# Kernel tuning notes

Hardware: AMD Instinct MI355X
Metric: run time of the kernel (lower is better)

The kernel has to match this reference:

```python
import jax, jax.numpy as jnp
import numpy as np

B, T, D, H, L, V = 4, 512, 512, 8, 8, 32000
HS = D // H
DF = 4 * D
EPS = 1e-5


def setup_inputs() -> dict:
    key = jax.random.key(0)
    ks = jax.random.split(key, 16)
    p = lambda k, s: jax.random.normal(k, s, jnp.float32) * 0.02
    return {
        'idx': jax.random.randint(ks[0], (B, T), 0, V),
        'targets': jax.random.randint(ks[1], (B, T), 0, V),
        'tok_emb': p(ks[2], (V, D)),
        'pos_emb': p(ks[3], (T, D)),
        'un_qkv_w': p(ks[4], (L, 3, D, D)),
        'un_qkv_b': jnp.zeros((L, 3, D), jnp.float32),
        'un_proj_w': p(ks[5], (L, D, D)),
        'un_proj_b': jnp.zeros((L, D), jnp.float32),
        'm_qkv_w': p(ks[6], (L, 3, D, D)),
        'm_qkv_b': jnp.zeros((L, 3, D), jnp.float32),
        'm_proj_w': p(ks[7], (L, D, D)),
        'm_proj_b': jnp.zeros((L, D), jnp.float32),
        'ff_w1': p(ks[8], (L, D, DF)),
        'ff_b1': jnp.zeros((L, DF), jnp.float32),
        'ff_w2': p(ks[9], (L, DF, D)),
        'ff_b2': jnp.zeros((L, D), jnp.float32),
        'ln1_g': jnp.ones((L, D), jnp.float32),
        'ln1_b': jnp.zeros((L, D), jnp.float32),
        'ln2_g': jnp.ones((L, D), jnp.float32),
        'ln2_b': jnp.zeros((L, D), jnp.float32),
        'lnf_g': jnp.ones((D,), jnp.float32),
        'lnf_b': jnp.zeros((D,), jnp.float32),
        'w_out': p(ks[10], (D, V)),
        'b_out': jnp.zeros((V,), jnp.float32),
    }


def _ln(x, g, b):
    mu = jnp.mean(x, -1, keepdims=True)
    var = jnp.var(x, -1, keepdims=True)
    return (x - mu) * jax.lax.rsqrt(var + EPS) * g + b


def _mha(x, qkv_w, qkv_b, pw, pb, mask):
    b, t, _ = x.shape
    # per-head linears concatenated == single D->D linear split into heads
    qkv = jnp.einsum('btd,cdf->cbtf', x, qkv_w) + qkv_b[:, None, None, :]
    q, k, v = (a.reshape(b, t, H, HS).transpose(0, 2, 1, 3) for a in qkv)
    w = jnp.einsum('bhtd,bhsd->bhts', q, k) * (HS ** -0.5)
    if mask is not None:
        w = jnp.where(mask, w, -jnp.inf)
    w = jax.nn.softmax(w, -1)  # dropout is identity in eval
    o = jnp.einsum('bhts,bhsd->bhtd', w, v).transpose(0, 2, 1, 3).reshape(b, t, D)
    return o @ pw + pb


def _ff(x, w1, b1, w2, b2):
    return jax.nn.gelu(x @ w1 + b1, approximate=False) @ w2 + b2


def _forward(idx, targets, tok_emb, pos_emb, layer_params, lnf_g, lnf_b, w_out, b_out):
    b, t = idx.shape
    x = tok_emb[idx] + pos_emb[:t]
    tril = jnp.tril(jnp.ones((t, t), bool))[None, None]

    def step(x, p):
        (uqw, uqb, upw, upb, mqw, mqb, mpw, mpb,
         w1, b1, w2, b2, g1, bb1, g2, bb2) = p
        # Block.forward (norm1/norm2/ffwd params are reused twice, as in source)
        x2 = x + _mha(_ln(x, g1, bb1), uqw, uqb, upw, upb, None)
        x = x2 + _ff(_ln(x2, g2, bb2), w1, b1, w2, b2)
        x2 = x + _mha(_ln(x, g1, bb1), mqw, mqb, mpw, mpb, tril)
        x = x2 + _ff(_ln(x2, g2, bb2), w1, b1, w2, b2)
        return x, None

    x, _ = jax.lax.scan(step, x, layer_params)
    x = _ln(x, lnf_g, lnf_b)
    logits = x @ w_out + b_out
    lsm = jax.nn.log_softmax(logits, -1)
    loss = -jnp.take_along_axis(lsm, targets[..., None], -1).mean()
    return logits, loss


def reference(idx, targets, tok_emb, pos_emb, un_qkv_w, un_qkv_b, un_proj_w,
              un_proj_b, m_qkv_w, m_qkv_b, m_proj_w, m_proj_b, ff_w1, ff_b1,
              ff_w2, ff_b2, ln1_g, ln1_b, ln2_g, ln2_b, lnf_g, lnf_b, w_out,
              b_out):
    layer_params = (un_qkv_w, un_qkv_b, un_proj_w, un_proj_b, m_qkv_w, m_qkv_b,
                    m_proj_w, m_proj_b, ff_w1, ff_b1, ff_w2, ff_b2, ln1_g,
                    ln1_b, ln2_g, ln2_b)
    return _forward(idx, targets, tok_emb, pos_emb, layer_params, lnf_g,
                    lnf_b, w_out, b_out)
```

## Files before the change

kernel.cpp:

```cpp
#include <hip/hip_runtime.h>

typedef unsigned short u16;
typedef __bf16 bf16x8 __attribute__((ext_vector_type(8)));
typedef float f32x4 __attribute__((ext_vector_type(4)));
typedef u16 u16x8 __attribute__((ext_vector_type(8)));

#define DEVINL __device__ __forceinline__

static constexpr int Tn  = 512;
static constexpr int Dn  = 512;
static constexpr int Hn  = 8;
static constexpr int HSn = 64;
static constexpr int Vn  = 32000;
static constexpr int Lnum = 8;
static constexpr int DFn = 2048;
static constexpr int BTn = 2048;

DEVINL u16 f2bf(float f) {
  unsigned u = __float_as_uint(f);
  u += 0x7fffu + ((u >> 16) & 1u);
  return (u16)(u >> 16);
}

DEVINL void gl_lds16(const u16* src, u16* dst) {
  __builtin_amdgcn_global_load_lds(
      (const __attribute__((address_space(1))) unsigned int*)src,
      (__attribute__((address_space(3))) unsigned int*)dst, 16, 0, 0);
}

__global__ __launch_bounds__(256) void transpose_w(const float* __restrict__ in,
                                                   u16* __restrict__ out,
                                                   int R, int C) {
  __shared__ float tile[32][33];
  long zoff = (long)blockIdx.z * R * C;
  int c0 = blockIdx.x * 32, r0 = blockIdx.y * 32;
  for (int e = threadIdx.x; e < 1024; e += 256) {
    int r = e >> 5, c = e & 31;
    tile[r][c] = in[zoff + (long)(r0 + r) * C + (c0 + c)];
  }
  __syncthreads();
  for (int e = threadIdx.x; e < 1024; e += 256) {
    int c = e >> 5, r = e & 31;
    out[zoff + (long)(c0 + c) * R + (r0 + r)] = f2bf(tile[r][c]);
  }
}

__global__ __launch_bounds__(256) void embed_kernel(const int* __restrict__ idx,
                                                    const float* __restrict__ tok,
                                                    const float* __restrict__ pos,
                                                    float* __restrict__ x) {
  int i = blockIdx.x * 256 + threadIdx.x;
  int bt = i >> 7;
  int d4 = (i & 127) * 4;
  int t = bt & (Tn - 1);
  long tk = (long)idx[bt] * Dn + d4;
  f32x4 a = *(const f32x4*)(tok + tk);
  f32x4 p = *(const f32x4*)(pos + (long)t * Dn + d4);
  a = a + p;
  *(f32x4*)(x + (long)bt * Dn + d4) = a;
}

__global__ __launch_bounds__(256) void ln_kernel(const float* __restrict__ x,
                                                 const float* __restrict__ g,
                                                 const float* __restrict__ b,
                                                 u16* __restrict__ out) {
  int lane = threadIdx.x & 63, wid = threadIdx.x >> 6;
  long row = (long)blockIdx.x * 4 + wid;
  const float* xr = x + row * Dn;
  f32x4 v0 = *(const f32x4*)(xr + lane * 8);
  f32x4 v1 = *(const f32x4*)(xr + lane * 8 + 4);
  float s = v0[0] + v0[1] + v0[2] + v0[3] + v1[0] + v1[1] + v1[2] + v1[3];
  float s2 = v0[0]*v0[0] + v0[1]*v0[1] + v0[2]*v0[2] + v0[3]*v0[3]
           + v1[0]*v1[0] + v1[1]*v1[1] + v1[2]*v1[2] + v1[3]*v1[3];
#pragma unroll
  for (int o = 32; o; o >>= 1) { s += __shfl_xor(s, o); s2 += __shfl_xor(s2, o); }
  float mu = s * (1.f / Dn);
  float rv = rsqrtf(s2 * (1.f / Dn) - mu * mu + 1e-5f);
  u16x8 o8;
#pragma unroll
  for (int j = 0; j < 8; ++j) {
    int c = lane * 8 + j;
    float xv = (j < 4) ? v0[j] : v1[j - 4];
    o8[j] = f2bf((xv - mu) * rv * g[c] + b[c]);
  }
  *(u16x8*)(out + row * Dn + lane * 8) = o8;
}

template<int BM, int BN, bool BIAS, bool RES, bool GELU, bool OBF, bool LOSSP>
__global__ __launch_bounds__(256, 2)
void gemm_kernel(const u16* __restrict__ A, const u16* __restrict__ B,
                 const float* __restrict__ bias, const float* __restrict__ res,
                 void* __restrict__ Cptr, int M, int N, int K, int ldc,
                 long aBatch, long bBatch, int zdiv, long zs1, long zs2,
                 float* __restrict__ lossP) {
  constexpr int BK = 32;
  constexpr int FM = BM / 32, FN = BN / 32;
  __shared__ __align__(16) u16 lds[2][(BM + BN) * BK];
  const int tid = threadIdx.x, lane = tid & 63, wid = tid >> 6;
  const int z = blockIdx.z;
  const u16* Ab = A + (long)z * aBatch + (long)blockIdx.y * BM * K;
  const u16* Bb = B + (long)z * bBatch + (long)blockIdx.x * BN * K;
  const int wr = wid >> 1, wc = wid & 1;
  const int r16 = lane & 15, kg = lane >> 4;

  f32x4 acc[FM][FN];
#pragma unroll
  for (int i = 0; i < FM; ++i)
#pragma unroll
    for (int j = 0; j < FN; ++j) acc[i][j] = (f32x4){0.f, 0.f, 0.f, 0.f};

  auto stage = [&](int buf, int kt) {
#pragma unroll
    for (int i = 0; i < BM / 64; ++i) {
      int fr = i * 4 + wid;
      const u16* src = Ab + (long)(fr * 16 + r16) * K + kt * BK + kg * 8;
      gl_lds16(src, &lds[buf][(i * 4 + wid) * 512]);
    }
#pragma unroll
    for (int i = 0; i < BN / 64; ++i) {
      int fr = i * 4 + wid;
      const u16* src = Bb + (long)(fr * 16 + r16) * K + kt * BK + kg * 8;
      gl_lds16(src, &lds[buf][BM * BK + (i * 4 + wid) * 512]);
    }
  };

  const int NT = K / BK;
  stage(0, 0);
  int cur = 0;
  for (int kt = 0; kt < NT; ++kt) {
    __syncthreads();
    if (kt + 1 < NT) stage(cur ^ 1, kt + 1);
    const u16* la = &lds[cur][0];
    const u16* lb = &lds[cur][BM * BK];
    bf16x8 af[FM], bfr[FN];
#pragma unroll
    for (int mi = 0; mi < FM; ++mi)
      af[mi] = *(const bf16x8*)(la + ((wr * FM + mi) * 64 + lane) * 8);
#pragma unroll
    for (int ni = 0; ni < FN; ++ni)
      bfr[ni] = *(const bf16x8*)(lb + ((wc * FN + ni) * 64 + lane) * 8);
#pragma unroll
    for (int mi = 0; mi < FM; ++mi)
#pragma unroll
      for (int ni = 0; ni < FN; ++ni)
        acc[mi][ni] = __builtin_amdgcn_mfma_f32_16x16x32_bf16(
            af[mi], bfr[ni], acc[mi][ni], 0, 0, 0);
    cur ^= 1;
  }

  if (LOSSP) {
#pragma unroll
    for (int mi = 0; mi < FM; ++mi) {
      float vals[FN][4];
#pragma unroll
      for (int ni = 0; ni < FN; ++ni) {
        int col = blockIdx.x * BN + wc * (BN / 2) + ni * 16 + r16;
        float bv = bias[col];
#pragma unroll
        for (int r = 0; r < 4; ++r) {
          int row = blockIdx.y * BM + wr * (BM / 2) + mi * 16 + kg * 4 + r;
          float v = acc[mi][ni][r] + bv;
          ((float*)Cptr)[(long)row * ldc + col] = v;
          vals[ni][r] = v;
        }
      }
#pragma unroll
      for (int r = 0; r < 4; ++r) {
        float mx = vals[0][r];
#pragma unroll
        for (int ni = 1; ni < FN; ++ni) mx = fmaxf(mx, vals[ni][r]);
#pragma unroll
        for (int off = 1; off < 16; off <<= 1) mx = fmaxf(mx, __shfl_xor(mx, off));
        float s = 0.f;
#pragma unroll
        for (int ni = 0; ni < FN; ++ni) s += __expf(vals[ni][r] - mx);
#pragma unroll
        for (int off = 1; off < 16; off <<= 1) s += __shfl_xor(s, off);
        if (r16 == 0) {
          int row = blockIdx.y * BM + wr * (BM / 2) + mi * 16 + kg * 4 + r;
          int grp = blockIdx.x * (BN / 64) + wc;
          float2* pp = (float2*)lossP;
          pp[(long)row * (Vn / 64) + grp] = make_float2(mx, s);
        }
      }
    }
    return;
  }

  long cOff = (long)(z / zdiv) * zs1 + (long)(z % zdiv) * zs2;
#pragma unroll
  for (int mi = 0; mi < FM; ++mi) {
#pragma unroll
    for (int ni = 0; ni < FN; ++ni) {
      int col = blockIdx.x * BN + wc * (BN / 2) + ni * 16 + r16;
      float bv = 0.f;
      if (BIAS) bv = bias[col];
#pragma unroll
      for (int r = 0; r < 4; ++r) {
        int row = blockIdx.y * BM + wr * (BM / 2) + mi * 16 + kg * 4 + r;
        float v = acc[mi][ni][r] + bv;
        if (GELU) v = 0.5f * v * (1.f + erff(v * 0.70710678f));
        long ci = cOff + (long)row * ldc + col;
        if (RES) v += res[ci];
        if (OBF) ((u16*)Cptr)[ci] = f2bf(v);
        else     ((float*)Cptr)[ci] = v;
      }
    }
  }
}

__global__ __launch_bounds__(256) void qkv_split(const u16* __restrict__ qkv,
                                                 u16* __restrict__ q,
                                                 u16* __restrict__ k,
                                                 u16* __restrict__ vT) {
  __shared__ u16 vt[32][72];
  int bh = blockIdx.y, b = bh >> 3, h = bh & 7;
  int t0 = blockIdx.x * 32;
  for (int e = threadIdx.x; e < 2048; e += 256) {
    int tt = e >> 6, d = e & 63;
    long src = ((long)(b * Tn + t0 + tt)) * (3 * Dn) + h * HSn + d;
    long dst = ((long)bh * Tn + t0 + tt) * HSn + d;
    q[dst] = qkv[src];
    k[dst] = qkv[src + Dn];
    vt[tt][d] = qkv[src + 2 * Dn];
  }
  __syncthreads();
  for (int e = threadIdx.x; e < 2048; e += 256) {
    int d = e >> 5, tt = e & 31;
    vT[((long)bh * HSn + d) * Tn + t0 + tt] = vt[tt][d];
  }
}

template<int CAUSAL>
__global__ __launch_bounds__(256, 2)
void flash_kernel(const u16* __restrict__ qb, const u16* __restrict__ kb,
                  const u16* __restrict__ vTb, u16* __restrict__ ob) {
  __shared__ __align__(16) u16 Qs[8 * 512];
  __shared__ __align__(16) u16 Ks[16 * 512];
  __shared__ __align__(16) u16 Vs[16 * 512];
  __shared__ __align__(16) u16 Ps[16 * 512];
  const int tid = threadIdx.x, lane = tid & 63, w = tid >> 6;
  const int r16 = lane & 15, kg = lane >> 4;
  const int bh = blockIdx.y, qt = blockIdx.x, q0 = qt * 64;
  const long bhT = (long)bh * Tn;

#pragma unroll
  for (int ks = 0; ks < 2; ++ks) {
    const u16* src = qb + (bhT + q0 + w * 16 + r16) * 64 + ks * 32 + kg * 8;
    gl_lds16(src, Qs + (ks * 4 + w) * 512);
  }

  f32x4 acc_o[4];
#pragma unroll
  for (int fd = 0; fd < 4; ++fd) acc_o[fd] = (f32x4){0.f, 0.f, 0.f, 0.f};
  float m[4], l[4];
#pragma unroll
  for (int r = 0; r < 4; ++r) { m[r] = -1e30f; l[r] = 0.f; }

  const int nt = CAUSAL ? (qt >> 1) + 1 : 4;
  for (int it = 0; it < nt; ++it) {
    const int kt0 = it * 128;
    __syncthreads();
#pragma unroll
    for (int j = 0; j < 4; ++j) {
      int idx = j * 4 + w;
      int ks = idx >> 3, fn = idx & 7;
      const u16* src = kb + (bhT + kt0 + fn * 16 + r16) * 64 + ks * 32 + kg * 8;
      gl_lds16(src, Ks + idx * 512);
    }
#pragma unroll
    for (int j = 0; j < 4; ++j) {
      int idx = j * 4 + w;
      int ks = idx >> 2, fn = idx & 3;
      const u16* src = vTb + ((long)bh * 64 + fn * 16 + r16) * 512 + kt0 + ks * 32 + kg * 8;
      gl_lds16(src, Vs + idx * 512);
    }
    __syncthreads();

    f32x4 sa[8];
#pragma unroll
    for (int fn = 0; fn < 8; ++fn) sa[fn] = (f32x4){0.f, 0.f, 0.f, 0.f};
#pragma unroll
    for (int ks = 0; ks < 2; ++ks) {
      bf16x8 aq = *(const bf16x8*)(Qs + (ks * 4 + w) * 512 + lane * 8);
#pragma unroll
      for (int fn = 0; fn < 8; ++fn)
        sa[fn] = __builtin_amdgcn_mfma_f32_16x16x32_bf16(
            aq, *(const bf16x8*)(Ks + (ks * 8 + fn) * 512 + lane * 8), sa[fn], 0, 0, 0);
    }

    const bool masked = CAUSAL && (it == nt - 1);
#pragma unroll
    for (int r = 0; r < 4; ++r) {
      float sv[8];
      float mx = -1e30f;
      int qv = q0 + w * 16 + kg * 4 + r;
#pragma unroll
      for (int fn = 0; fn < 8; ++fn) {
        float vv = sa[fn][r] * 0.125f;
        if (masked) {
          int ktv = kt0 + fn * 16 + r16;
          if (ktv > qv) vv = -1e30f;
        }
        sv[fn] = vv;
        mx = fmaxf(mx, vv);
      }
#pragma unroll
      for (int off = 1; off < 16; off <<= 1) mx = fmaxf(mx, __shfl_xor(mx, off));
      float nm = fmaxf(m[r], mx);
      float sc = __expf(m[r] - nm);
      float rs = 0.f;
#pragma unroll
      for (int fn = 0; fn < 8; ++fn) { float p = __expf(sv[fn] - nm); sv[fn] = p; rs += p; }
#pragma unroll
      for (int off = 1; off < 16; off <<= 1) rs += __shfl_xor(rs, off);
      l[r] = l[r] * sc + rs;
      m[r] = nm;
#pragma unroll
      for (int fd = 0; fd < 4; ++fd) acc_o[fd][r] *= sc;
#pragma unroll
      for (int fn = 0; fn < 8; ++fn) {
        int t = fn * 16 + r16;
        int q = kg * 4 + r;
        Ps[w * 2048 + (t >> 5) * 512 + ((t >> 3) & 3) * 128 + q * 8 + (t & 7)] = f2bf(sv[fn]);
      }
    }

#pragma unroll
    for (int ks = 0; ks < 4; ++ks) {
      bf16x8 pa = *(const bf16x8*)(Ps + w * 2048 + ks * 512 + lane * 8);
#pragma unroll
      for (int fd = 0; fd < 4; ++fd)
        acc_o[fd] = __builtin_amdgcn_mfma_f32_16x16x32_bf16(
            pa, *(const bf16x8*)(Vs + (ks * 4 + fd) * 512 + lane * 8), acc_o[fd], 0, 0, 0);
    }
  }

  const int b = bh >> 3, h = bh & 7;
#pragma unroll
  for (int fd = 0; fd < 4; ++fd) {
#pragma unroll
    for (int r = 0; r < 4; ++r) {
      int q = q0 + w * 16 + kg * 4 + r;
      int d = fd * 16 + r16;
      ob[((long)(b * Tn + q)) * Dn + h * 64 + d] = f2bf(acc_o[fd][r] / l[r]);
    }
  }
}

__global__ __launch_bounds__(256) void loss_combine(const float* __restrict__ lossP,
                                                    const float* __restrict__ logits,
                                                    const int* __restrict__ targets,
                                                    float* __restrict__ loss) {
  int w = threadIdx.x >> 6, lane = threadIdx.x & 63;
  int row = blockIdx.x * 4 + w;
  const float2* lp = (const float2*)lossP + (long)row * (Vn / 64);
  float m = -1e30f, s = 0.f;
  for (int e = lane; e < Vn / 64; e += 64) {
    float2 p = lp[e];
    float nm = fmaxf(m, p.x);
    s = s * __expf(m - nm) + p.y * __expf(p.x - nm);
    m = nm;
  }
#pragma unroll
  for (int off = 1; off < 64; off <<= 1) {
    float om = __shfl_xor(m, off), os = __shfl_xor(s, off);
    float nm = fmaxf(m, om);
    s = s * __expf(m - nm) + os * __expf(om - nm);
    m = nm;
  }
  if (lane == 0) {
    float lse = m + logf(s);
    float nll = lse - logits[(long)row * Vn + targets[row]];
    atomicAdd(loss, nll * (1.f / BTn));
  }
}

extern "C" void kernel_launch(void* const* d_in, const int* in_sizes, int n_in,
                              void* d_out, int out_size, void* d_ws, size_t ws_size,
                              hipStream_t stream) {
  const int*   idx      = (const int*)d_in[0];
  const int*   targets  = (const int*)d_in[1];
  const float* tok_emb  = (const float*)d_in[2];
  const float* pos_emb  = (const float*)d_in[3];
  const float* un_qkv_w = (const float*)d_in[4];
  const float* un_qkv_b = (const float*)d_in[5];
  const float* un_proj_w= (const float*)d_in[6];
  const float* un_proj_b= (const float*)d_in[7];
  const float* m_qkv_w  = (const float*)d_in[8];
  const float* m_qkv_b  = (const float*)d_in[9];
  const float* m_proj_w = (const float*)d_in[10];
  const float* m_proj_b = (const float*)d_in[11];
  const float* ff_w1    = (const float*)d_in[12];
  const float* ff_b1    = (const float*)d_in[13];
  const float* ff_w2    = (const float*)d_in[14];
  const float* ff_b2    = (const float*)d_in[15];
  const float* ln1_g    = (const float*)d_in[16];
  const float* ln1_b    = (const float*)d_in[17];
  const float* ln2_g    = (const float*)d_in[18];
  const float* ln2_b    = (const float*)d_in[19];
  const float* lnf_g    = (const float*)d_in[20];
  const float* lnf_b    = (const float*)d_in[21];
  const float* w_out    = (const float*)d_in[22];
  const float* b_out    = (const float*)d_in[23];

  char* wsp = (char*)d_ws;
  auto alloc = [&](size_t bytes) -> void* {
    void* p = (void*)wsp;
    wsp += (bytes + 255) & ~(size_t)255;
    return p;
  };
  u16* unqkvT = (u16*)alloc((size_t)Lnum * 3 * Dn * Dn * 2);
  u16* mqkvT  = (u16*)alloc((size_t)Lnum * 3 * Dn * Dn * 2);
  u16* unprojT= (u16*)alloc((size_t)Lnum * Dn * Dn * 2);
  u16* mprojT = (u16*)alloc((size_t)Lnum * Dn * Dn * 2);
  u16* ff1T   = (u16*)alloc((size_t)Lnum * Dn * DFn * 2);
  u16* ff2T   = (u16*)alloc((size_t)Lnum * DFn * Dn * 2);
  u16* woutT  = (u16*)alloc((size_t)Dn * Vn * 2);
  float* x    = (float*)alloc((size_t)BTn * Dn * 4);
  float* x2   = (float*)alloc((size_t)BTn * Dn * 4);
  u16* xn     = (u16*)alloc((size_t)BTn * Dn * 2);
  u16* qb     = (u16*)alloc((size_t)32 * Tn * HSn * 2);
  u16* kb     = (u16*)alloc((size_t)32 * Tn * HSn * 2);
  u16* vT     = (u16*)alloc((size_t)32 * HSn * Tn * 2);
  u16* ob     = (u16*)alloc((size_t)BTn * Dn * 2);
  u16* scr    = (u16*)alloc((size_t)BTn * DFn * 2);
  float* lossP= (float*)alloc((size_t)BTn * (Vn / 64) * 8);
  u16* qkvb = scr;
  u16* hb   = scr;

  dim3 blk(256);

  transpose_w<<<dim3(16, 16, 24), blk, 0, stream>>>(un_qkv_w, unqkvT, Dn, Dn);
  transpose_w<<<dim3(16, 16, 24), blk, 0, stream>>>(m_qkv_w,  mqkvT,  Dn, Dn);
  transpose_w<<<dim3(16, 16, 8),  blk, 0, stream>>>(un_proj_w, unprojT, Dn, Dn);
  transpose_w<<<dim3(16, 16, 8),  blk, 0, stream>>>(m_proj_w,  mprojT,  Dn, Dn);
  transpose_w<<<dim3(64, 16, 8),  blk, 0, stream>>>(ff_w1, ff1T, Dn, DFn);
  transpose_w<<<dim3(16, 64, 8),  blk, 0, stream>>>(ff_w2, ff2T, DFn, Dn);
  transpose_w<<<dim3(1000, 16, 1),blk, 0, stream>>>(w_out, woutT, Dn, Vn);

  embed_kernel<<<dim3(BTn * Dn / 4 / 256), blk, 0, stream>>>(idx, tok_emb, pos_emb, x);

  auto run_mha = [&](const float* xin, float* xout, const u16* qkvT_l,
                     const float* qkvb_l, const u16* projT_l, const float* projb_l,
                     const float* g1, const float* b1, int causal) {
    ln_kernel<<<dim3(BTn / 4), blk, 0, stream>>>(xin, g1, b1, xn);
    gemm_kernel<128, 128, true, false, false, true, false>
        <<<dim3(12, 16, 1), blk, 0, stream>>>(xn, qkvT_l, qkvb_l, nullptr, qkvb,
            BTn, 3 * Dn, Dn, 3 * Dn, 0, 0, 1, 0, 0, nullptr);
    qkv_split<<<dim3(Tn / 32, 32), blk, 0, stream>>>(qkvb, qb, kb, vT);
    if (causal)
      flash_kernel<1><<<dim3(8, 32), blk, 0, stream>>>(qb, kb, vT, ob);
    else
      flash_kernel<0><<<dim3(8, 32), blk, 0, stream>>>(qb, kb, vT, ob);
    gemm_kernel<64, 128, true, true, false, false, false>
        <<<dim3(4, 32, 1), blk, 0, stream>>>(ob, projT_l, projb_l, xin, xout,
            BTn, Dn, Dn, Dn, 0, 0, 1, 0, 0, nullptr);
  };

  auto run_ff = [&](const float* xin, float* xout, const u16* w1T_l,
                    const float* b1_l, const u16* w2T_l, const float* b2_l,
                    const float* g2, const float* bb2) {
    ln_kernel<<<dim3(BTn / 4), blk, 0, stream>>>(xin, g2, bb2, xn);
    gemm_kernel<128, 128, true, false, true, true, false>
        <<<dim3(16, 16, 1), blk, 0, stream>>>(xn, w1T_l, b1_l, nullptr, hb,
            BTn, DFn, Dn, DFn, 0, 0, 1, 0, 0, nullptr);
    gemm_kernel<64, 128, true, true, false, false, false>
        <<<dim3(4, 32, 1), blk, 0, stream>>>(hb, w2T_l, b2_l, xin, xout,
            BTn, Dn, DFn, Dn, 0, 0, 1, 0, 0, nullptr);
  };

  for (int l = 0; l < Lnum; ++l) {
    const u16* uqT = unqkvT + (size_t)l * 3 * Dn * Dn;
    const u16* mqT = mqkvT  + (size_t)l * 3 * Dn * Dn;
    const u16* upT = unprojT+ (size_t)l * Dn * Dn;
    const u16* mpT = mprojT + (size_t)l * Dn * Dn;
    const u16* w1T = ff1T   + (size_t)l * Dn * DFn;
    const u16* w2T = ff2T   + (size_t)l * DFn * Dn;
    const float* g1 = ln1_g + l * Dn, *bb1 = ln1_b + l * Dn;
    const float* g2 = ln2_g + l * Dn, *bb2 = ln2_b + l * Dn;

    run_mha(x, x2, uqT, un_qkv_b + l * 3 * Dn, upT, un_proj_b + l * Dn, g1, bb1, 0);
    run_ff(x2, x, w1T, ff_b1 + l * DFn, w2T, ff_b2 + l * Dn, g2, bb2);
    run_mha(x, x2, mqT, m_qkv_b + l * 3 * Dn, mpT, m_proj_b + l * Dn, g1, bb1, 1);
    run_ff(x2, x, w1T, ff_b1 + l * DFn, w2T, ff_b2 + l * Dn, g2, bb2);
  }

  ln_kernel<<<dim3(BTn / 4), blk, 0, stream>>>(x, lnf_g, lnf_b, xn);
  float* logits = (float*)d_out;
  gemm_kernel<128, 128, true, false, false, false, true>
      <<<dim3(Vn / 128, 16, 1), blk, 0, stream>>>(xn, woutT, b_out, nullptr, logits,
          BTn, Vn, Dn, Vn, 0, 0, 1, 0, 0, lossP);
  float* loss_ptr = logits + (size_t)BTn * Vn;
  hipMemsetAsync((void*)loss_ptr, 0, 4, stream);
  loss_combine<<<dim3(BTn / 4), blk, 0, stream>>>(lossP, logits, targets, loss_ptr);
}
```

Measured before the change: 2.438 ms.

## Fuse QKV head-split into GEMM epilogue and retune GEMM tiles and occupancy

The QKV GEMM epilogue now writes Q, K and V directly in per-head layout, so the separate split kernel shrinks to a V-only transpose and the intermediate QKV buffer round-trip goes away. Per-layer GEMMs move to smaller tiles (64x128, 64x64) with higher minimum-waves launch bounds, giving more blocks on the many CUs. The logits GEMM grid is swapped so M-blocks vary fastest, improving reuse of the output weight tiles in cache. The scattered bf16 epilogue stores and tighter register budget could lower store efficiency or cause spills.

```diff
diff --git a/kernel.cpp b/kernel.cpp
--- a/kernel.cpp
+++ b/kernel.cpp
@@ -86,20 +86,22 @@
   *(u16x8*)(out + row * Dn + lane * 8) = o8;
 }
 
-template<int BM, int BN, bool BIAS, bool RES, bool GELU, bool OBF, bool LOSSP>
-__global__ __launch_bounds__(256, 2)
+template<int BM, int BN, int MINW, bool BIAS, bool RES, bool GELU, bool OBF,
+         bool LOSSP, bool QKV>
+__global__ __launch_bounds__(256, MINW)
 void gemm_kernel(const u16* __restrict__ A, const u16* __restrict__ B,
                  const float* __restrict__ bias, const float* __restrict__ res,
                  void* __restrict__ Cptr, int M, int N, int K, int ldc,
-                 long aBatch, long bBatch, int zdiv, long zs1, long zs2,
-                 float* __restrict__ lossP) {
+                 float* __restrict__ lossP,
+                 u16* __restrict__ qp, u16* __restrict__ kp, u16* __restrict__ vp) {
   constexpr int BK = 32;
   constexpr int FM = BM / 32, FN = BN / 32;
   __shared__ __align__(16) u16 lds[2][(BM + BN) * BK];
   const int tid = threadIdx.x, lane = tid & 63, wid = tid >> 6;
-  const int z = blockIdx.z;
-  const u16* Ab = A + (long)z * aBatch + (long)blockIdx.y * BM * K;
-  const u16* Bb = B + (long)z * bBatch + (long)blockIdx.x * BN * K;
+  const int bxc = LOSSP ? blockIdx.y : blockIdx.x;
+  const int byr = LOSSP ? blockIdx.x : blockIdx.y;
+  const u16* Ab = A + (long)byr * BM * K;
+  const u16* Bb = B + (long)bxc * BN * K;
   const int wr = wid >> 1, wc = wid & 1;
   const int r16 = lane & 15, kg = lane >> 4;
 
@@ -148,17 +150,40 @@
     cur ^= 1;
   }
 
+  if (QKV) {
+#pragma unroll
+    for (int mi = 0; mi < FM; ++mi) {
+#pragma unroll
+      for (int ni = 0; ni < FN; ++ni) {
+        int col = bxc * BN + wc * (BN / 2) + ni * 16 + r16;
+        float bv = bias[col];
+        int cls = col >> 9, h = (col >> 6) & 7, d = col & 63;
+#pragma unroll
+        for (int r = 0; r < 4; ++r) {
+          int row = byr * BM + wr * (BM / 2) + mi * 16 + kg * 4 + r;
+          int b = row >> 9, t = row & 511;
+          long a = ((long)(b * 8 + h) * Tn + t) * HSn + d;
+          u16 ov = f2bf(acc[mi][ni][r] + bv);
+          if (cls == 0) qp[a] = ov;
+          else if (cls == 1) kp[a] = ov;
+          else vp[a] = ov;
+        }
+      }
+    }
+    return;
+  }
+
   if (LOSSP) {
 #pragma unroll
     for (int mi = 0; mi < FM; ++mi) {
       float vals[FN][4];
 #pragma unroll
       for (int ni = 0; ni < FN; ++ni) {
-        int col = blockIdx.x * BN + wc * (BN / 2) + ni * 16 + r16;
+        int col = bxc * BN + wc * (BN / 2) + ni * 16 + r16;
         float bv = bias[col];
 #pragma unroll
         for (int r = 0; r < 4; ++r) {
-          int row = blockIdx.y * BM + wr * (BM / 2) + mi * 16 + kg * 4 + r;
+          int row = byr * BM + wr * (BM / 2) + mi * 16 + kg * 4 + r;
           float v = acc[mi][ni][r] + bv;
           ((float*)Cptr)[(long)row * ldc + col] = v;
           vals[ni][r] = v;
@@ -177,30 +202,28 @@
 #pragma unroll
         for (int off = 1; off < 16; off <<= 1) s += __shfl_xor(s, off);
         if (r16 == 0) {
-          int row = blockIdx.y * BM + wr * (BM / 2) + mi * 16 + kg * 4 + r;
-          int grp = blockIdx.x * (BN / 64) + wc;
-          float2* pp = (float2*)lossP;
-          pp[(long)row * (Vn / 64) + grp] = make_float2(mx, s);
+          int row = byr * BM + wr * (BM / 2) + mi * 16 + kg * 4 + r;
+          int grp = bxc * (BN / 64) + wc;
+          ((float2*)lossP)[(long)row * (Vn / 64) + grp] = make_float2(mx, s);
         }
       }
     }
     return;
   }
 
-  long cOff = (long)(z / zdiv) * zs1 + (long)(z % zdiv) * zs2;
 #pragma unroll
   for (int mi = 0; mi < FM; ++mi) {
 #pragma unroll
     for (int ni = 0; ni < FN; ++ni) {
-      int col = blockIdx.x * BN + wc * (BN / 2) + ni * 16 + r16;
+      int col = bxc * BN + wc * (BN / 2) + ni * 16 + r16;
       float bv = 0.f;
       if (BIAS) bv = bias[col];
 #pragma unroll
       for (int r = 0; r < 4; ++r) {
-        int row = blockIdx.y * BM + wr * (BM / 2) + mi * 16 + kg * 4 + r;
+        int row = byr * BM + wr * (BM / 2) + mi * 16 + kg * 4 + r;
         float v = acc[mi][ni][r] + bv;
         if (GELU) v = 0.5f * v * (1.f + erff(v * 0.70710678f));
-        long ci = cOff + (long)row * ldc + col;
+        long ci = (long)row * ldc + col;
         if (RES) v += res[ci];
         if (OBF) ((u16*)Cptr)[ci] = f2bf(v);
         else     ((float*)Cptr)[ci] = v;
@@ -209,20 +232,14 @@
   }
 }
 
-__global__ __launch_bounds__(256) void qkv_split(const u16* __restrict__ qkv,
-                                                 u16* __restrict__ q,
-                                                 u16* __restrict__ k,
-                                                 u16* __restrict__ vT) {
+__global__ __launch_bounds__(256) void vtrans(const u16* __restrict__ vtmp,
+                                              u16* __restrict__ vT) {
   __shared__ u16 vt[32][72];
-  int bh = blockIdx.y, b = bh >> 3, h = bh & 7;
+  int bh = blockIdx.y;
   int t0 = blockIdx.x * 32;
   for (int e = threadIdx.x; e < 2048; e += 256) {
     int tt = e >> 6, d = e & 63;
-    long src = ((long)(b * Tn + t0 + tt)) * (3 * Dn) + h * HSn + d;
-    long dst = ((long)bh * Tn + t0 + tt) * HSn + d;
-    q[dst] = qkv[src];
-    k[dst] = qkv[src + Dn];
-    vt[tt][d] = qkv[src + 2 * Dn];
+    vt[tt][d] = vtmp[((long)bh * Tn + t0 + tt) * HSn + d];
   }
   __syncthreads();
   for (int e = threadIdx.x; e < 2048; e += 256) {
@@ -422,12 +439,11 @@
   u16* xn     = (u16*)alloc((size_t)BTn * Dn * 2);
   u16* qb     = (u16*)alloc((size_t)32 * Tn * HSn * 2);
   u16* kb     = (u16*)alloc((size_t)32 * Tn * HSn * 2);
+  u16* vtmp   = (u16*)alloc((size_t)32 * Tn * HSn * 2);
   u16* vT     = (u16*)alloc((size_t)32 * HSn * Tn * 2);
   u16* ob     = (u16*)alloc((size_t)BTn * Dn * 2);
-  u16* scr    = (u16*)alloc((size_t)BTn * DFn * 2);
+  u16* hb     = (u16*)alloc((size_t)BTn * DFn * 2);
   float* lossP= (float*)alloc((size_t)BTn * (Vn / 64) * 8);
-  u16* qkvb = scr;
-  u16* hb   = scr;
 
   dim3 blk(256);
 
@@ -445,29 +461,29 @@
                      const float* qkvb_l, const u16* projT_l, const float* projb_l,
                      const float* g1, const float* b1, int causal) {
     ln_kernel<<<dim3(BTn / 4), blk, 0, stream>>>(xin, g1, b1, xn);
-    gemm_kernel<128, 128, true, false, false, true, false>
-        <<<dim3(12, 16, 1), blk, 0, stream>>>(xn, qkvT_l, qkvb_l, nullptr, qkvb,
-            BTn, 3 * Dn, Dn, 3 * Dn, 0, 0, 1, 0, 0, nullptr);
-    qkv_split<<<dim3(Tn / 32, 32), blk, 0, stream>>>(qkvb, qb, kb, vT);
+    gemm_kernel<64, 128, 4, true, false, false, false, false, true>
+        <<<dim3(12, 32), blk, 0, stream>>>(xn, qkvT_l, qkvb_l, nullptr, nullptr,
+            BTn, 3 * Dn, Dn, 0, nullptr, qb, kb, vtmp);
+    vtrans<<<dim3(Tn / 32, 32), blk, 0, stream>>>(vtmp, vT);
     if (causal)
       flash_kernel<1><<<dim3(8, 32), blk, 0, stream>>>(qb, kb, vT, ob);
     else
       flash_kernel<0><<<dim3(8, 32), blk, 0, stream>>>(qb, kb, vT, ob);
-    gemm_kernel<64, 128, true, true, false, false, false>
-        <<<dim3(4, 32, 1), blk, 0, stream>>>(ob, projT_l, projb_l, xin, xout,
-            BTn, Dn, Dn, Dn, 0, 0, 1, 0, 0, nullptr);
+    gemm_kernel<64, 64, 4, true, true, false, false, false, false>
+        <<<dim3(8, 32), blk, 0, stream>>>(ob, projT_l, projb_l, xin, xout,
+            BTn, Dn, Dn, Dn, nullptr, nullptr, nullptr, nullptr);
   };
 
   auto run_ff = [&](const float* xin, float* xout, const u16* w1T_l,
                     const float* b1_l, const u16* w2T_l, const float* b2_l,
                     const float* g2, const float* bb2) {
     ln_kernel<<<dim3(BTn / 4), blk, 0, stream>>>(xin, g2, bb2, xn);
-    gemm_kernel<128, 128, true, false, true, true, false>
-        <<<dim3(16, 16, 1), blk, 0, stream>>>(xn, w1T_l, b1_l, nullptr, hb,
-            BTn, DFn, Dn, DFn, 0, 0, 1, 0, 0, nullptr);
-    gemm_kernel<64, 128, true, true, false, false, false>
-        <<<dim3(4, 32, 1), blk, 0, stream>>>(hb, w2T_l, b2_l, xin, xout,
-            BTn, Dn, DFn, Dn, 0, 0, 1, 0, 0, nullptr);
+    gemm_kernel<64, 128, 4, true, false, true, true, false, false>
+        <<<dim3(16, 32), blk, 0, stream>>>(xn, w1T_l, b1_l, nullptr, hb,
+            BTn, DFn, Dn, DFn, nullptr, nullptr, nullptr, nullptr);
+    gemm_kernel<64, 64, 4, true, true, false, false, false, false>
+        <<<dim3(8, 32), blk, 0, stream>>>(hb, w2T_l, b2_l, xin, xout,
+            BTn, Dn, DFn, Dn, nullptr, nullptr, nullptr, nullptr);
   };
 
   for (int l = 0; l < Lnum; ++l) {
@@ -488,9 +504,9 @@
 
   ln_kernel<<<dim3(BTn / 4), blk, 0, stream>>>(x, lnf_g, lnf_b, xn);
   float* logits = (float*)d_out;
-  gemm_kernel<128, 128, true, false, false, false, true>
-      <<<dim3(Vn / 128, 16, 1), blk, 0, stream>>>(xn, woutT, b_out, nullptr, logits,
-          BTn, Vn, Dn, Vn, 0, 0, 1, 0, 0, lossP);
+  gemm_kernel<128, 128, 3, true, false, false, false, true, false>
+      <<<dim3(16, Vn / 128), blk, 0, stream>>>(xn, woutT, b_out, nullptr, logits,
+          BTn, Vn, Dn, Vn, lossP, nullptr, nullptr, nullptr);
   float* loss_ptr = logits + (size_t)BTn * Vn;
   hipMemsetAsync((void*)loss_ptr, 0, 4, stream);
   loss_combine<<<dim3(BTn / 4), blk, 0, stream>>>(lossP, logits, targets, loss_ptr);
```

Result: faster. 2.199 ms (-9.8%).
